# Optimization experiments

Measured on AMD Instinct MI355X. Metric: run time of the kernel, lower is better.

## Reference

```python
import jax, jax.numpy as jnp
import numpy as np
from jax import lax

VOCAB = 50000; EMB = 128; HID = 256; NL = 9; B = 128; T = 512; H = HID // 2; PAD = 0


def setup_inputs() -> dict:
    key = jax.random.key(0)
    ks = jax.random.split(key, 16)
    p = lambda k, s: jax.random.normal(k, s, jnp.float32) * 0.05
    return {
        "chars": jax.random.randint(ks[0], (B, T), 1, VOCAB),  # in [1, VOCAB) so mask fully on
        "labels": jax.random.randint(ks[1], (B, T), 0, NL),
        "emb": p(ks[2], (VOCAB, EMB)),
        "W_ih_f": p(ks[3], (4 * H, EMB)), "W_hh_f": p(ks[4], (4 * H, H)),
        "b_ih_f": p(ks[5], (4 * H,)), "b_hh_f": p(ks[6], (4 * H,)),
        "W_ih_b": p(ks[7], (4 * H, EMB)), "W_hh_b": p(ks[8], (4 * H, H)),
        "b_ih_b": p(ks[9], (4 * H,)), "b_hh_b": p(ks[10], (4 * H,)),
        "W_out": p(ks[11], (NL, HID)), "b_out": p(ks[12], (NL,)),
        "start_trans": p(ks[13], (NL,)), "end_trans": p(ks[14], (NL,)),
        "trans": p(ks[15], (NL, NL)),
    }


def _lstm(x, Wih, Whh, bih, bhh, reverse):
    # x: (B, T, D); PyTorch gate order i, f, g, o
    bsz = x.shape[0]
    h0 = jnp.zeros((bsz, H), x.dtype)
    c0 = jnp.zeros((bsz, H), x.dtype)
    b = bih + bhh

    def step(carry, xt):
        h, c = carry
        g = xt @ Wih.T + h @ Whh.T + b  # (B, 4H)
        i, f, gg, o = jnp.split(g, 4, axis=-1)
        c = jax.nn.sigmoid(f) * c + jax.nn.sigmoid(i) * jnp.tanh(gg)
        h = jax.nn.sigmoid(o) * jnp.tanh(c)
        return (h, c), h

    _, hs = lax.scan(step, (h0, c0), jnp.swapaxes(x, 0, 1), reverse=reverse)
    return jnp.swapaxes(hs, 0, 1)  # (B, T, H)


def _crf_nll(emissions, labels, mask, start, end, trans):
    # torchcrf linear-chain CRF log-likelihood, reduction='sum'
    maskf = mask.astype(emissions.dtype)
    emit = jnp.take_along_axis(emissions, labels[..., None], 2)[..., 0]  # (B, T)
    score = start[labels[:, 0]] + (emit * maskf).sum(1)
    score = score + (trans[labels[:, :-1], labels[:, 1:]] * maskf[:, 1:]).sum(1)
    last_idx = mask.sum(1).astype(jnp.int32) - 1
    last_tags = jnp.take_along_axis(labels, last_idx[:, None], 1)[:, 0]
    score = score + end[last_tags]

    # forward algorithm (log partition) as a scan over time
    alpha0 = start[None, :] + emissions[:, 0]  # (B, L)

    def step(alpha, inp):
        e_t, m_t = inp  # (B, L), (B,)
        nxt = jax.nn.logsumexp(alpha[:, :, None] + trans[None, :, :], axis=1) + e_t
        return jnp.where(m_t[:, None], nxt, alpha), None

    alpha, _ = lax.scan(step, alpha0,
                        (jnp.swapaxes(emissions, 0, 1)[1:], jnp.swapaxes(mask, 0, 1)[1:]))
    logZ = jax.nn.logsumexp(alpha + end[None, :], axis=-1)
    return -(score - logZ).sum()


def reference(chars, labels, emb, W_ih_f, W_hh_f, b_ih_f, b_hh_f,
              W_ih_b, W_hh_b, b_ih_b, b_hh_b, W_out, b_out,
              start_trans, end_trans, trans):
    x = emb[chars]  # (B, T, EMB)
    hf = _lstm(x, W_ih_f, W_hh_f, b_ih_f, b_hh_f, False)
    hb = _lstm(x, W_ih_b, W_hh_b, b_ih_b, b_hh_b, True)
    h = jnp.concatenate([hf, hb], axis=-1)  # (B, T, HID)
    emissions = h @ W_out.T + b_out  # dropout is identity in eval mode
    mask = chars != PAD
    return _crf_nll(emissions, labels, mask, start_trans, end_trans, trans)
```

## Files before the change

### kernel.cpp

```cpp
#include <hip/hip_runtime.h>

#define B_   128
#define T_   512
#define EMB_ 128
#define H_   128
#define NL_  9
#define MT_  65536

typedef __attribute__((ext_vector_type(8))) short short8v;
typedef __attribute__((ext_vector_type(4))) float float4v;

__device__ inline unsigned short f2bf(float f){
  unsigned u = __float_as_uint(f);
  u += 0x7FFFu + ((u >> 16) & 1u);
  return (unsigned short)(u >> 16);
}
__device__ inline float bf2f(unsigned short s){
  return __uint_as_float(((unsigned)s) << 16);
}
__device__ inline float sigm(float x){ return 1.f / (1.f + __expf(-x)); }
__device__ inline float tanh_(float x){ return 2.f / (1.f + __expf(-2.f * x)) - 1.f; }

#define LOG2E 1.44269504f
__device__ inline float vexp2(float x){ float r; asm("v_exp_f32 %0, %1" : "=v"(r) : "v"(x)); return r; }
__device__ inline float vrcp (float x){ float r; asm("v_rcp_f32 %0, %1" : "=v"(r) : "v"(x)); return r; }
__device__ inline float sigmf_(float x){
  return vrcp(1.f + vexp2(-LOG2E * x));
}
__device__ inline float tanhf_(float x){
  return fmaf(2.f, vrcp(1.f + vexp2(-2.f * LOG2E * x)), -1.f);
}

__device__ inline void gload16(const void* g, void* l){
  __builtin_amdgcn_global_load_lds(
      (const __attribute__((address_space(1))) void*)g,
      (__attribute__((address_space(3)))       void*)l, 16, 0, 0);
}

__global__ void k0_prep(const float* __restrict__ Wihf, const float* __restrict__ Whhf,
                        const float* __restrict__ bihf, const float* __restrict__ bhhf,
                        const float* __restrict__ Wihb, const float* __restrict__ Whhb,
                        const float* __restrict__ bihb, const float* __restrict__ bhhb,
                        unsigned short* __restrict__ Wih2, unsigned short* __restrict__ Whh2,
                        float* __restrict__ biasc){
  int blk = blockIdx.x;
  int dir = blk >> 9;
  int nd  = blk & 511;
  int k   = threadIdx.x;
  int j = nd >> 2, g = nd & 3;
  int orig = g * 128 + j;
  const float* Wih = dir ? Wihb : Wihf;
  const float* Whh = dir ? Whhb : Whhf;
  Wih2[((long)(dir * 512 + nd)) * 128 + k] = f2bf(Wih[orig * EMB_ + k]);
  Whh2[((long)(dir * 512 + nd)) * 128 + k] = f2bf(Whh[orig * H_ + k]);
  if (k == 0){
    const float* bi = dir ? bihb : bihf;
    const float* bh = dir ? bhhb : bhhf;
    biasc[dir * 512 + nd] = bi[orig] + bh[orig];
  }
}

__global__ void k1_embed(const int* __restrict__ chars, const float* __restrict__ emb,
                         unsigned short* __restrict__ x){
  int i = blockIdx.x * blockDim.x + threadIdx.x;
  int m = i >> 5, q = i & 31;
  int c = chars[m];
  const float4* e4 = (const float4*)(emb + (long)c * EMB_);
  float4 v = e4[q];
  ushort4 o;
  o.x = f2bf(v.x); o.y = f2bf(v.y); o.z = f2bf(v.z); o.w = f2bf(v.w);
  *(ushort4*)(x + (long)m * EMB_ + q * 4) = o;
}

#define CST 130
__global__ __launch_bounds__(256) void k2_gemm(const unsigned short* __restrict__ x,
                                               const unsigned short* __restrict__ Wih2,
                                               const float* __restrict__ biasc,
                                               unsigned short* __restrict__ G){
  __shared__ unsigned short gsm[64 * CST];
  int w = threadIdx.x >> 6, lane = threadIdx.x & 63;
  int r = lane & 15, kb = (lane >> 4) * 8;
  long arow = (long)(blockIdx.x * 64 + w * 16 + r);
  short8v a[4];
  #pragma unroll
  for (int kf = 0; kf < 4; kf++)
    a[kf] = *(const short8v*)(x + arow * EMB_ + kf * 32 + kb);
  int ncol0 = blockIdx.y * 128;
  float4v acc[8];
  #pragma unroll
  for (int nf = 0; nf < 8; nf++){
    float4v z = {0.f, 0.f, 0.f, 0.f};
    acc[nf] = z;
    int wrow = ncol0 + nf * 16 + r;
    #pragma unroll
    for (int kf = 0; kf < 4; kf++){
      short8v bfrag = *(const short8v*)(Wih2 + (long)wrow * 128 + kf * 32 + kb);
      acc[nf] = __builtin_amdgcn_mfma_f32_16x16x32_bf16(a[kf], bfrag, acc[nf], 0, 0, 0);
    }
  }
  int rloc0 = w * 16 + (lane >> 4) * 4;
  #pragma unroll
  for (int nf = 0; nf < 8; nf++){
    int col = ncol0 + nf * 16 + r;
    float bia = biasc[col];
    #pragma unroll
    for (int reg = 0; reg < 4; reg++)
      gsm[(rloc0 + reg) * CST + nf * 16 + r] = f2bf(acc[nf][reg] + bia);
  }
  __syncthreads();
  #pragma unroll
  for (int it = 0; it < 4; it++){
    int u = it * 256 + threadIdx.x;
    int row = u >> 4, cu = u & 15;
    short8v v = *(const short8v*)&gsm[row * CST + cu * 8];
    *(short8v*)(G + (long)(blockIdx.x * 64 + row) * 1024 + ncol0 + cu * 8) = v;
  }
}

#define ASTR  136
#define GSTR  520
#define HBSTR 136
__global__ __launch_bounds__(512, 2) void k3_scan2(
    const unsigned short* __restrict__ G,
    const unsigned short* __restrict__ Whh2,
    unsigned short* __restrict__ hs)
{
  const int blk = blockIdx.x;
  const int dir = blk >> 3;
  const int b0  = (blk & 7) * 16;
  const int tid = threadIdx.x;
  const int w   = tid >> 6;
  const int l   = tid & 63;
  const int r   = l & 15;
  const int q   = l >> 4;
  const int jcol = w * 16 + r;

  __shared__ unsigned short hA[2][16 * ASTR];
  __shared__ unsigned short Gl[2][16 * GSTR];
  __shared__ unsigned short hbuf[8][16 * HBSTR];

  short8v Bf[4][4];
  #pragma unroll
  for (int g = 0; g < 4; g++){
    const unsigned short* wp = Whh2 + ((long)(dir * 512 + jcol * 4 + g)) * 128 + q * 8;
    #pragma unroll
    for (int kf = 0; kf < 4; kf++)
      Bf[g][kf] = *(const short8v*)(wp + kf * 32);
  }
  #pragma unroll
  for (int g = 0; g < 4; g++){
    #pragma unroll
    for (int kf = 0; kf < 4; kf++)
      asm volatile("" : "+v"(Bf[g][kf]));
  }

  for (int i = tid; i < 16 * ASTR; i += 512) hA[0][i] = 0;

  float cc[4] = {0.f, 0.f, 0.f, 0.f};
  const int hAoff = (jcol >> 3) * ASTR + (jcol & 7);

  {
    int t0 = dir ? (T_ - 1) : 0;
    #pragma unroll
    for (int i = 0; i < 2; i++){
      int row = 2 * w + i;
      const unsigned short* src = G + ((long)(b0 + row) * T_ + t0) * 1024 + dir * 512 + l * 8;
      gload16(src, &Gl[0][row * GSTR]);
    }
  }
  __syncthreads();

  for (int s = 0; s < T_; s++){
    const int p = s & 1;
    if (s + 1 < T_){
      int tn = dir ? (T_ - 2 - s) : (s + 1);
      #pragma unroll
      for (int i = 0; i < 2; i++){
        int row = 2 * w + i;
        const unsigned short* src = G + ((long)(b0 + row) * T_ + tn) * 1024 + dir * 512 + l * 8;
        gload16(src, &Gl[p ^ 1][row * GSTR]);
      }
    }

    float4v acc[4];
    #pragma unroll
    for (int g = 0; g < 4; g++){ float4v z = {0.f,0.f,0.f,0.f}; acc[g] = z; }
    #pragma unroll
    for (int kf = 0; kf < 4; kf++){
      short8v af = *(const short8v*)&hA[p][(kf * 4 + q) * ASTR + r * 8];
      #pragma unroll
      for (int g = 0; g < 4; g++)
        acc[g] = __builtin_amdgcn_mfma_f32_16x16x32_bf16(af, Bf[g][kf], acc[g], 0, 0, 0);
    }

    #pragma unroll
    for (int reg = 0; reg < 4; reg++){
      int m = q * 4 + reg;
      ushort4 gp = *(const ushort4*)&Gl[p][m * GSTR + jcol * 4];
      float iv = sigmf_(acc[0][reg] + bf2f(gp.x));
      float fv = sigmf_(acc[1][reg] + bf2f(gp.y));
      float gg = tanhf_(acc[2][reg] + bf2f(gp.z));
      float ov = sigmf_(acc[3][reg] + bf2f(gp.w));
      cc[reg] = fv * cc[reg] + iv * gg;
      float hv = ov * tanhf_(cc[reg]);
      unsigned short hb = f2bf(hv);
      hA[p ^ 1][hAoff + m * 8] = hb;
      hbuf[s & 7][m * HBSTR + jcol] = hb;
    }
    __syncthreads();

    if ((s & 7) == 7){
      #pragma unroll
      for (int mr = 0; mr < 4; mr++){
        int u  = tid + mr * 512;
        int j8 = u & 15, mm = (u >> 4) & 15, ii = u >> 8;
        int sg = s - 7 + ii;
        int tg = dir ? (T_ - 1 - sg) : sg;
        short8v v = *(const short8v*)&hbuf[ii][mm * HBSTR + j8 * 8];
        *(short8v*)(hs + ((long)dir * MT_ + (long)(b0 + mm) * T_ + tg) * H_ + j8 * 8) = v;
      }
      __syncthreads();
    }
  }
}

#define HSTR 264
__global__ __launch_bounds__(512) void k4_emis(const unsigned short* __restrict__ hs,
                                               const float* __restrict__ Wout,
                                               const float* __restrict__ bout,
                                               float* __restrict__ em){
  __shared__ float hcat[64 * HSTR];
  __shared__ float wo[NL_ * 256];
  int tid = threadIdx.x;
  int m0 = blockIdx.x * 64;
  const unsigned short* hf = hs;
  const unsigned short* hb = hs + (long)MT_ * H_;
  #pragma unroll
  for (int it = 0; it < 8; it++){
    int flat = it * 2048 + tid * 4;
    int r = flat >> 8, u = flat & 255;
    const unsigned short* src = (u < 128) ? (hf + (long)(m0 + r) * H_ + u)
                                          : (hb + (long)(m0 + r) * H_ + (u - 128));
    ushort4 v = *(const ushort4*)src;
    hcat[r * HSTR + u]     = bf2f(v.x);
    hcat[r * HSTR + u + 1] = bf2f(v.y);
    hcat[r * HSTR + u + 2] = bf2f(v.z);
    hcat[r * HSTR + u + 3] = bf2f(v.w);
  }
  for (int f = tid; f < NL_ * 256; f += 512) wo[f] = Wout[f];
  __syncthreads();
  #pragma unroll
  for (int half = 0; half < 2; half++){
    int idx = half * 512 + tid;
    if (idx < 64 * NL_){
      int r = idx / NL_, lbl = idx % NL_;
      float acc = bout[lbl];
      #pragma unroll 8
      for (int u = 0; u < 256; u++)
        acc = fmaf(hcat[r * HSTR + u], wo[lbl * 256 + u], acc);
      em[(long)(m0 + r) * NL_ + lbl] = acc;
    }
  }
}

__global__ void k5_crf(const float* __restrict__ em, const int* __restrict__ chars,
                       const int* __restrict__ labels, const float* __restrict__ startv,
                       const float* __restrict__ endv, const float* __restrict__ trans,
                       float* __restrict__ partial){
  int b = blockIdx.x, lane = threadIdx.x;
  const int* lab = labels + b * T_;
  const int* ch  = chars + b * T_;
  const float* e = em + (long)b * T_ * NL_;
  float sc = 0.f; int cnt = 0;
  for (int t = lane; t < T_; t += 64){
    int m = (ch[t] != 0);
    cnt += m;
    if (m){
      sc += e[t * NL_ + lab[t]];
      if (t > 0) sc += trans[lab[t - 1] * NL_ + lab[t]];
    }
  }
  #pragma unroll
  for (int off = 32; off; off >>= 1){
    sc  += __shfl_down(sc, off);
    cnt += __shfl_down(cnt, off);
  }
  sc  = __shfl(sc, 0);
  cnt = __shfl(cnt, 0);
  if (cnt < 1) cnt = 1;
  int jl = (lane < NL_) ? lane : 0;
  float tcol[NL_];
  #pragma unroll
  for (int i = 0; i < NL_; i++) tcol[i] = trans[i * NL_ + jl];
  float alpha = (lane < NL_) ? (startv[jl] + e[jl]) : -1e30f;
  float evn = (lane < NL_) ? e[NL_ + jl] : 0.f;
  int   mn  = (ch[1] != 0);
  for (int t = 1; t < T_; t++){
    float ev = evn; int m = mn;
    int t2 = (t + 1 < T_) ? t + 1 : t;
    evn = (lane < NL_) ? e[t2 * NL_ + jl] : 0.f;
    mn  = (ch[t2] != 0);
    float vv[NL_]; float mx = -1e30f;
    #pragma unroll
    for (int i = 0; i < NL_; i++){
      vv[i] = __shfl(alpha, i) + tcol[i];
      mx = fmaxf(mx, vv[i]);
    }
    float ssum = 0.f;
    #pragma unroll
    for (int i = 0; i < NL_; i++) ssum += __expf(vv[i] - mx);
    float nxt = mx + __logf(ssum) + ev;
    if (m && lane < NL_) alpha = nxt;
  }
  float av = (lane < NL_) ? (alpha + endv[jl]) : -1e30f;
  float mx = av;
  #pragma unroll
  for (int off = 8; off; off >>= 1) mx = fmaxf(mx, __shfl_down(mx, off));
  mx = __shfl(mx, 0);
  float ex = (lane < NL_) ? __expf(av - mx) : 0.f;
  #pragma unroll
  for (int off = 8; off; off >>= 1) ex += __shfl_down(ex, off);
  if (lane == 0){
    float logZ = mx + __logf(ex);
    float score = sc + startv[lab[0]] + endv[lab[cnt - 1]];
    partial[b] = logZ - score;
  }
}

__global__ void k6_reduce(const float* __restrict__ partial, float* __restrict__ out){
  int lane = threadIdx.x;
  float v = partial[lane];
  #pragma unroll
  for (int off = 32; off; off >>= 1) v += __shfl_down(v, off);
  __shared__ float tmp[2];
  if ((lane & 63) == 0) tmp[lane >> 6] = v;
  __syncthreads();
  if (lane == 0) out[0] = tmp[0] + tmp[1];
}

extern "C" void kernel_launch(void* const* d_in, const int* in_sizes, int n_in,
                              void* d_out, int out_size, void* d_ws, size_t ws_size,
                              hipStream_t stream){
  const int*   chars  = (const int*)d_in[0];
  const int*   labels = (const int*)d_in[1];
  const float* emb    = (const float*)d_in[2];
  const float* Wihf   = (const float*)d_in[3];
  const float* Whhf   = (const float*)d_in[4];
  const float* bihf   = (const float*)d_in[5];
  const float* bhhf   = (const float*)d_in[6];
  const float* Wihb   = (const float*)d_in[7];
  const float* Whhb   = (const float*)d_in[8];
  const float* bihb   = (const float*)d_in[9];
  const float* bhhb   = (const float*)d_in[10];
  const float* Wout   = (const float*)d_in[11];
  const float* bout   = (const float*)d_in[12];
  const float* startv = (const float*)d_in[13];
  const float* endv   = (const float*)d_in[14];
  const float* trans  = (const float*)d_in[15];

  char* ws = (char*)d_ws;
  unsigned short* x     = (unsigned short*)(ws);
  float*          em    = (float*)         (ws);
  float*          part  = (float*)         (ws + 2359296);
  unsigned short* Wih2  = (unsigned short*)(ws + 16777216);
  unsigned short* Whh2  = (unsigned short*)(ws + 17301504);
  float*          biasc = (float*)         (ws + 17825792);
  unsigned short* G     = (unsigned short*)(ws + 17829888);
  unsigned short* hs    = (unsigned short*)(ws + 152047616);

  hipLaunchKernelGGL(k0_prep,  dim3(1024), dim3(128), 0, stream,
                     Wihf, Whhf, bihf, bhhf, Wihb, Whhb, bihb, bhhb, Wih2, Whh2, biasc);
  hipLaunchKernelGGL(k1_embed, dim3(8192), dim3(256), 0, stream, chars, emb, x);
  hipLaunchKernelGGL(k2_gemm,  dim3(1024, 8), dim3(256), 0, stream, x, Wih2, biasc, G);
  hipLaunchKernelGGL(k3_scan2, dim3(16),   dim3(512), 0, stream, G, Whh2, hs);
  hipLaunchKernelGGL(k4_emis,  dim3(1024), dim3(512), 0, stream, hs, Wout, bout, em);
  hipLaunchKernelGGL(k5_crf,   dim3(128),  dim3(64),  0, stream,
                     em, chars, labels, startv, endv, trans, part);
  hipLaunchKernelGGL(k6_reduce, dim3(1),   dim3(128), 0, stream, part, (float*)d_out);
}
```

Before: 973.9 us.

## Restructure LSTM scan to 1024-thread blocks with transposed MFMA and fused cell math

The recurrent scan kernel now runs 16 waves per block instead of 8, and each wave computes two 16-gate MFMA tiles. The weights are the A operand and h is the B operand, so each lane ends up holding all four gates of one hidden unit. The precomputed input projection is loaded straight into the accumulators, which removes the separate add. The LSTM cell math is fused so that it uses fewer reciprocals, and h is packed with a single cvt_pk instruction. A 4-deep ring buffer replaces the separate hA/hbuf buffers and is flushed to global memory every 4 steps. The aim is to shorten the serial per-step latency of the recurrence. The cost is more barrier participants per step and fewer VGPRs available per thread.

```diff
diff --git a/kernel.cpp b/kernel.cpp
--- a/kernel.cpp
+++ b/kernel.cpp
@@ -24,11 +24,19 @@
 #define LOG2E 1.44269504f
 __device__ inline float vexp2(float x){ float r; asm("v_exp_f32 %0, %1" : "=v"(r) : "v"(x)); return r; }
 __device__ inline float vrcp (float x){ float r; asm("v_rcp_f32 %0, %1" : "=v"(r) : "v"(x)); return r; }
-__device__ inline float sigmf_(float x){
-  return vrcp(1.f + vexp2(-LOG2E * x));
-}
-__device__ inline float tanhf_(float x){
-  return fmaf(2.f, vrcp(1.f + vexp2(-2.f * LOG2E * x)), -1.f);
+
+__device__ inline float lstm_cell(float pi, float pf, float pg, float po, float& c){
+  float ei = vexp2(-LOG2E * pi);
+  float ef = vexp2(-LOG2E * pf);
+  float eg = vexp2( 2.f * LOG2E * pg);
+  float eo = vexp2(-LOG2E * po);
+  float R1 = vrcp((1.f + ei) * (1.f + eg));
+  float ig = (eg - 1.f) * R1;
+  float F  = vrcp(1.f + ef);
+  c = fmaf(F, c, ig);
+  float ec = vexp2(2.f * LOG2E * c);
+  float R2 = vrcp((1.f + eo) * (1.f + ec));
+  return (ec - 1.f) * R2;
 }
 
 __device__ inline void gload16(const void* g, void* l){
@@ -117,10 +125,9 @@
   }
 }
 
-#define ASTR  136
-#define GSTR  520
-#define HBSTR 136
-__global__ __launch_bounds__(512, 2) void k3_scan2(
+#define HBST 136
+#define GSTR 520
+__global__ __launch_bounds__(1024, 1) void k3_scan3(
     const unsigned short* __restrict__ G,
     const unsigned short* __restrict__ Whh2,
     unsigned short* __restrict__ hs)
@@ -133,92 +140,76 @@
   const int l   = tid & 63;
   const int r   = l & 15;
   const int q   = l >> 4;
-  const int jcol = w * 16 + r;
-
-  __shared__ unsigned short hA[2][16 * ASTR];
+
+  __shared__ unsigned short hR[4][16 * HBST];
   __shared__ unsigned short Gl[2][16 * GSTR];
-  __shared__ unsigned short hbuf[8][16 * HBSTR];
-
-  short8v Bf[4][4];
-  #pragma unroll
-  for (int g = 0; g < 4; g++){
-    const unsigned short* wp = Whh2 + ((long)(dir * 512 + jcol * 4 + g)) * 128 + q * 8;
+
+  short8v Wf[2][4];
+  #pragma unroll
+  for (int t = 0; t < 2; t++){
+    const unsigned short* wp = Whh2 + ((long)(dir * 512 + 32 * w + 16 * t + r)) * 128 + q * 8;
     #pragma unroll
     for (int kf = 0; kf < 4; kf++)
-      Bf[g][kf] = *(const short8v*)(wp + kf * 32);
-  }
-  #pragma unroll
-  for (int g = 0; g < 4; g++){
-    #pragma unroll
-    for (int kf = 0; kf < 4; kf++)
-      asm volatile("" : "+v"(Bf[g][kf]));
-  }
-
-  for (int i = tid; i < 16 * ASTR; i += 512) hA[0][i] = 0;
-
-  float cc[4] = {0.f, 0.f, 0.f, 0.f};
-  const int hAoff = (jcol >> 3) * ASTR + (jcol & 7);
-
-  {
-    int t0 = dir ? (T_ - 1) : 0;
-    #pragma unroll
-    for (int i = 0; i < 2; i++){
-      int row = 2 * w + i;
-      const unsigned short* src = G + ((long)(b0 + row) * T_ + t0) * 1024 + dir * 512 + l * 8;
-      gload16(src, &Gl[0][row * GSTR]);
-    }
-  }
+      Wf[t][kf] = *(const short8v*)(wp + kf * 32);
+  }
+
+  for (int i = tid; i < 16 * HBST; i += 1024) hR[3][i] = 0;
+
+  float cc0 = 0.f, cc1 = 0.f;
+  const int j0 = 8 * w + q;
+  const int j1 = j0 + 4;
+
+  const unsigned short* Gp0 = G + ((long)(b0 + w) * T_ + (dir ? T_ - 1 : 0)) * 1024
+                                + dir * 512 + l * 8;
+  const long gstep = (dir ? -1L : 1L) * 1024;
+  const unsigned short* Gp = Gp0 + gstep;
+
+  gload16(Gp0, &Gl[0][w * GSTR]);
   __syncthreads();
 
   for (int s = 0; s < T_; s++){
     const int p = s & 1;
     if (s + 1 < T_){
-      int tn = dir ? (T_ - 2 - s) : (s + 1);
-      #pragma unroll
-      for (int i = 0; i < 2; i++){
-        int row = 2 * w + i;
-        const unsigned short* src = G + ((long)(b0 + row) * T_ + tn) * 1024 + dir * 512 + l * 8;
-        gload16(src, &Gl[p ^ 1][row * GSTR]);
-      }
-    }
-
-    float4v acc[4];
-    #pragma unroll
-    for (int g = 0; g < 4; g++){ float4v z = {0.f,0.f,0.f,0.f}; acc[g] = z; }
-    #pragma unroll
-    for (int kf = 0; kf < 4; kf++){
-      short8v af = *(const short8v*)&hA[p][(kf * 4 + q) * ASTR + r * 8];
-      #pragma unroll
-      for (int g = 0; g < 4; g++)
-        acc[g] = __builtin_amdgcn_mfma_f32_16x16x32_bf16(af, Bf[g][kf], acc[g], 0, 0, 0);
-    }
-
-    #pragma unroll
-    for (int reg = 0; reg < 4; reg++){
-      int m = q * 4 + reg;
-      ushort4 gp = *(const ushort4*)&Gl[p][m * GSTR + jcol * 4];
-      float iv = sigmf_(acc[0][reg] + bf2f(gp.x));
-      float fv = sigmf_(acc[1][reg] + bf2f(gp.y));
-      float gg = tanhf_(acc[2][reg] + bf2f(gp.z));
-      float ov = sigmf_(acc[3][reg] + bf2f(gp.w));
-      cc[reg] = fv * cc[reg] + iv * gg;
-      float hv = ov * tanhf_(cc[reg]);
-      unsigned short hb = f2bf(hv);
-      hA[p ^ 1][hAoff + m * 8] = hb;
-      hbuf[s & 7][m * HBSTR + jcol] = hb;
-    }
+      gload16(Gp, &Gl[p ^ 1][w * GSTR]);
+      Gp += gstep;
+    }
+
+    const unsigned short* hrow = &hR[(s + 3) & 3][r * HBST + q * 8];
+    short8v hf0 = *(const short8v*)(hrow);
+    short8v hf1 = *(const short8v*)(hrow + 32);
+    short8v hf2 = *(const short8v*)(hrow + 64);
+    short8v hf3 = *(const short8v*)(hrow + 96);
+
+    ushort4 gp0 = *(const ushort4*)&Gl[p][r * GSTR + 32 * w + 4 * q];
+    ushort4 gp1 = *(const ushort4*)&Gl[p][r * GSTR + 32 * w + 16 + 4 * q];
+    float4v acc0 = {bf2f(gp0.x), bf2f(gp0.y), bf2f(gp0.z), bf2f(gp0.w)};
+    float4v acc1 = {bf2f(gp1.x), bf2f(gp1.y), bf2f(gp1.z), bf2f(gp1.w)};
+
+    acc0 = __builtin_amdgcn_mfma_f32_16x16x32_bf16(Wf[0][0], hf0, acc0, 0, 0, 0);
+    acc0 = __builtin_amdgcn_mfma_f32_16x16x32_bf16(Wf[0][1], hf1, acc0, 0, 0, 0);
+    acc0 = __builtin_amdgcn_mfma_f32_16x16x32_bf16(Wf[0][2], hf2, acc0, 0, 0, 0);
+    acc0 = __builtin_amdgcn_mfma_f32_16x16x32_bf16(Wf[0][3], hf3, acc0, 0, 0, 0);
+    acc1 = __builtin_amdgcn_mfma_f32_16x16x32_bf16(Wf[1][0], hf0, acc1, 0, 0, 0);
+    acc1 = __builtin_amdgcn_mfma_f32_16x16x32_bf16(Wf[1][1], hf1, acc1, 0, 0, 0);
+    acc1 = __builtin_amdgcn_mfma_f32_16x16x32_bf16(Wf[1][2], hf2, acc1, 0, 0, 0);
+    acc1 = __builtin_amdgcn_mfma_f32_16x16x32_bf16(Wf[1][3], hf3, acc1, 0, 0, 0);
+
+    float hv0 = lstm_cell(acc0[0], acc0[1], acc0[2], acc0[3], cc0);
+    float hv1 = lstm_cell(acc1[0], acc1[1], acc1[2], acc1[3], cc1);
+
+    unsigned pk;
+    asm("v_cvt_pk_bf16_f32 %0, %1, %2" : "=v"(pk) : "v"(hv0), "v"(hv1));
+    unsigned short* wrow = &hR[s & 3][r * HBST];
+    wrow[j0] = (unsigned short)pk;
+    wrow[j1] = (unsigned short)(pk >> 16);
     __syncthreads();
 
-    if ((s & 7) == 7){
-      #pragma unroll
-      for (int mr = 0; mr < 4; mr++){
-        int u  = tid + mr * 512;
-        int j8 = u & 15, mm = (u >> 4) & 15, ii = u >> 8;
-        int sg = s - 7 + ii;
-        int tg = dir ? (T_ - 1 - sg) : sg;
-        short8v v = *(const short8v*)&hbuf[ii][mm * HBSTR + j8 * 8];
-        *(short8v*)(hs + ((long)dir * MT_ + (long)(b0 + mm) * T_ + tg) * H_ + j8 * 8) = v;
-      }
+    if ((s & 3) == 3){
+      int ii = tid >> 8, mm = (tid >> 4) & 15, j8 = tid & 15;
+      int sg = s - 3 + ii;
+      int tg = dir ? (T_ - 1 - sg) : sg;
+      short8v v = *(const short8v*)&hR[ii][mm * HBST + j8 * 8];
+      *(short8v*)(hs + ((long)dir * MT_ + (long)(b0 + mm) * T_ + tg) * H_ + j8 * 8) = v;
       __syncthreads();
     }
   }
@@ -372,7 +363,7 @@
                      Wihf, Whhf, bihf, bhhf, Wihb, Whhb, bihb, bhhb, Wih2, Whh2, biasc);
   hipLaunchKernelGGL(k1_embed, dim3(8192), dim3(256), 0, stream, chars, emb, x);
   hipLaunchKernelGGL(k2_gemm,  dim3(1024, 8), dim3(256), 0, stream, x, Wih2, biasc, G);
-  hipLaunchKernelGGL(k3_scan2, dim3(16),   dim3(512), 0, stream, G, Whh2, hs);
+  hipLaunchKernelGGL(k3_scan3, dim3(16),   dim3(1024), 0, stream, G, Whh2, hs);
   hipLaunchKernelGGL(k4_emis,  dim3(1024), dim3(512), 0, stream, hs, Wout, bout, em);
   hipLaunchKernelGGL(k5_crf,   dim3(128),  dim3(64),  0, stream,
                      em, chars, labels, startv, endv, trans, part);
```

After: 957.8 us. About the same (-1.7%).
